# Kernel optimization log

Measured on AMD Instinct MI355X. Metric: run time of the kernel, lower is better.

Reference implementation:

```python
import jax, jax.numpy as jnp
import numpy as np

B, N, FEAT = 64, 1024, 3
HID, STATE, LAYERS, NTYPES = 64, 32, 2, 10


def setup_inputs() -> dict:
    key = jax.random.key(0)
    ks = jax.random.split(key, 16)
    s = 0.1
    return {
        "task_features": jax.random.normal(ks[0], (B, N, FEAT), jnp.float32),
        "task_types": jax.random.randint(ks[1], (B, N), 0, NTYPES, jnp.int32),
        "prev_state": jnp.zeros((B, STATE), jnp.float32),
        "enc_w1": jax.random.normal(ks[2], (HID, FEAT), jnp.float32) * s,
        "enc_b1": jnp.zeros((HID,), jnp.float32),
        "enc_w2": jax.random.normal(ks[3], (HID, HID), jnp.float32) * s,
        "enc_b2": jnp.zeros((HID,), jnp.float32),
        "contention": jax.random.normal(ks[4], (NTYPES, NTYPES), jnp.float32) * 0.1,
        "gnn_w": jax.random.normal(ks[5], (LAYERS, HID, HID), jnp.float32) * s,
        "gnn_b": jnp.zeros((LAYERS, HID), jnp.float32),
        "gru_w_ih": jax.random.normal(ks[6], (3 * STATE, HID), jnp.float32) * s,
        "gru_w_hh": jax.random.normal(ks[7], (3 * STATE, STATE), jnp.float32) * s,
        "gru_b_ih": jnp.zeros((3 * STATE,), jnp.float32),
        "gru_b_hh": jnp.zeros((3 * STATE,), jnp.float32),
        "head_w1": jax.random.normal(ks[8], (HID, HID + STATE), jnp.float32) * s,
        "head_b1": jnp.zeros((HID,), jnp.float32),
        "head_w2": jax.random.normal(ks[9], (1, HID), jnp.float32) * s,
        "head_b2": jnp.zeros((1,), jnp.float32),
    }


def _forward(task_features, task_types, prev_state, enc_w1, enc_b1, enc_w2, enc_b2,
             contention, gnn_w, gnn_b, gru_w_ih, gru_w_hh, gru_b_ih, gru_b_hh,
             head_w1, head_b1, head_w2, head_b2):
    # task encoder: Linear -> ReLU -> Linear
    emb = jax.nn.relu(task_features @ enc_w1.T + enc_b1) @ enc_w2.T + enc_b2  # (B,N,H)
    # interaction graph: type-pair gather + cosine similarity
    base = contention[task_types[:, :, None], task_types[:, None, :]]  # (B,N,N)
    nrm = emb / jnp.maximum(jnp.linalg.norm(emb, axis=-1, keepdims=True), 1e-12)
    sim = jnp.einsum("bnd,bmd->bnm", nrm, nrm)
    adjacency = jax.nn.sigmoid(base) * sim  # (B,N,N)
    # GNN layers: aggregate + linear + relu
    h = emb
    for l in range(LAYERS):
        agg = jnp.einsum("bnm,bmd->bnd", adjacency, h)
        h = jax.nn.relu((h + agg) @ gnn_w[l].T + gnn_b[l])
    ctx = h.mean(axis=1)  # (B,H)
    # GRUCell (torch semantics)
    gi = ctx @ gru_w_ih.T + gru_b_ih
    gh = prev_state @ gru_w_hh.T + gru_b_hh
    i_r, i_z, i_n = jnp.split(gi, 3, axis=-1)
    h_r, h_z, h_n = jnp.split(gh, 3, axis=-1)
    r = jax.nn.sigmoid(i_r + h_r)
    z = jax.nn.sigmoid(i_z + h_z)
    n = jnp.tanh(i_n + r * h_n)
    new_state = (1.0 - z) * n + z * prev_state  # (B,S)
    # latency head on [h, state]
    st = jnp.broadcast_to(new_state[:, None, :], (h.shape[0], h.shape[1], new_state.shape[-1]))
    combined = jnp.concatenate([h, st], axis=-1)
    lat = jax.nn.relu(combined @ head_w1.T + head_b1) @ head_w2.T + head_b2
    return lat[..., 0], new_state


def reference(task_features, task_types, prev_state, enc_w1, enc_b1, enc_w2, enc_b2,
              contention, gnn_w, gnn_b, gru_w_ih, gru_w_hh, gru_b_ih, gru_b_hh,
              head_w1, head_b1, head_w2, head_b2):
    return _forward(task_features, task_types, prev_state, enc_w1, enc_b1, enc_w2, enc_b2,
                    contention, gnn_w, gnn_b, gru_w_ih, gru_w_hh, gru_b_ih, gru_b_hh,
                    head_w1, head_b1, head_w2, head_b2)
```

## Files before the change

### kernel.cpp

```cpp
#include <hip/hip_runtime.h>
#include <math.h>

#define BB 64
#define NN 1024
#define HID 64
#define STATE 32
#define NTYPES 10

typedef _Float16 f16;
typedef f16 f16x8 __attribute__((ext_vector_type(8)));
typedef f16 f16x4 __attribute__((ext_vector_type(4)));
typedef float f32x4 __attribute__((ext_vector_type(4)));

#define MFMA16(a, b, c) __builtin_amdgcn_mfma_f32_16x16x32_f16(a, b, c, 0, 0, 0)

__device__ __forceinline__ float sigm(float x) { return 1.f / (1.f + expf(-x)); }

__device__ __forceinline__ f16x8 cvt8(float4 a, float4 b) {
    f16x8 r;
    r[0] = (f16)a.x; r[1] = (f16)a.y; r[2] = (f16)a.z; r[3] = (f16)a.w;
    r[4] = (f16)b.x; r[5] = (f16)b.y; r[6] = (f16)b.z; r[7] = (f16)b.w;
    return r;
}
__device__ __forceinline__ unsigned packh2(f16 a, f16 b) {
    union { f16 h[2]; unsigned u; } p;
    p.h[0] = a; p.h[1] = b;
    return p.u;
}

__global__ __launch_bounds__(256) void k_misc(
    const float* __restrict__ w2, const float* __restrict__ gw,
    const float* __restrict__ hw1, f16* __restrict__ out,
    int* __restrict__ cnt, float* __restrict__ ctx)
{
    int p = blockIdx.x * 256 + threadIdx.x;
    if (p < 18432) {
        const float* W; int K, pl;
        if (p < 12288) { int seg = p >> 12; pl = p & 4095; W = (seg == 0) ? w2 : gw + (seg - 1) * 4096; K = 64; }
        else { W = hw1; K = 96; pl = p - 12288; }
        int j = pl & 7, lane = (pl >> 3) & 63, nt = (pl >> 9) & 3, ch = pl >> 11;
        int k = ch * 32 + ((lane >> 4) << 3) + j;
        int o = nt * 16 + (lane & 15);
        out[p] = (f16)W[o * K + k];
        return;
    }
    int q = p - 18432;
    if (q < BB * NTYPES) { cnt[q] = 0; return; }
    q -= BB * NTYPES;
    if (q < BB * HID) ctx[q] = 0.f;
}

__global__ __launch_bounds__(256) void k_encoder(
    const float* __restrict__ feat,
    const float* __restrict__ w1, const float* __restrict__ b1,
    const f16* __restrict__ w2f, const float* __restrict__ b2,
    const int* __restrict__ types, int* __restrict__ idx, int* __restrict__ cnt,
    f16* __restrict__ nrm, float* __restrict__ sclv)
{
    __shared__ f16 w2s[4096];
    __shared__ f16 tmp[4][16 * 72];
    __shared__ float fbuf[4][48];
    int tid = threadIdx.x, wave = tid >> 6, lane = tid & 63;
    int l15 = lane & 15, quad = lane >> 4;
    if (tid < 64) {
        int row = blockIdx.x * 64 + tid;
        int b = row >> 10;
        int t = types[row];
        int pos = atomicAdd(&cnt[b * NTYPES + t], 1);
        idx[(b * NTYPES + t) * NN + pos] = row & (NN - 1);
    }
    { const uint4* s = (const uint4*)w2f; uint4* d = (uint4*)w2s;
      for (int i = tid; i < 512; i += 256) d[i] = s[i]; }
    float w10 = w1[lane * 3], w11 = w1[lane * 3 + 1], w12 = w1[lane * 3 + 2], b1l = b1[lane];
    int tb = blockIdx.x * 64 + wave * 16;
    if (lane < 48) fbuf[wave][lane] = feat[tb * 3 + lane];
    __syncthreads();
    f16* tw = &tmp[wave][0];
#pragma unroll
    for (int r = 0; r < 16; ++r) {
        float x0 = fbuf[wave][r * 3], x1 = fbuf[wave][r * 3 + 1], x2 = fbuf[wave][r * 3 + 2];
        float hv = fmaxf(fmaf(w10, x0, fmaf(w11, x1, fmaf(w12, x2, b1l))), 0.f);
        tw[r * 72 + lane] = (f16)hv;
    }
    __builtin_amdgcn_sched_barrier(0);
    f16x8 a0 = *(const f16x8*)&tw[l15 * 72 + quad * 8];
    f16x8 a1 = *(const f16x8*)&tw[l15 * 72 + 32 + quad * 8];
    const f16x8* bf = (const f16x8*)w2s;
    f32x4 acc[4];
#pragma unroll
    for (int nt = 0; nt < 4; ++nt) {
        f32x4 c = {0.f, 0.f, 0.f, 0.f};
        c = MFMA16(a0, bf[(0 * 4 + nt) * 64 + lane], c);
        c = MFMA16(a1, bf[(1 * 4 + nt) * 64 + lane], c);
        acc[nt] = c;
    }
    float b2c[4];
#pragma unroll
    for (int nt = 0; nt < 4; ++nt) b2c[nt] = b2[nt * 16 + l15];
#pragma unroll
    for (int i = 0; i < 4; ++i) {
        float v[4]; float ss = 0.f;
#pragma unroll
        for (int nt = 0; nt < 4; ++nt) { v[nt] = acc[nt][i] + b2c[nt]; ss = fmaf(v[nt], v[nt], ss); }
        ss += __shfl_xor(ss, 1, 64); ss += __shfl_xor(ss, 2, 64);
        ss += __shfl_xor(ss, 4, 64); ss += __shfl_xor(ss, 8, 64);
        float nm = fmaxf(sqrtf(ss), 1e-12f);
        float rinv = 1.f / nm;
        int grow = tb + quad * 4 + i;
#pragma unroll
        for (int nt = 0; nt < 4; ++nt)
            nrm[(size_t)grow * 64 + nt * 16 + l15] = (f16)(v[nt] * rinv);
        if (l15 == 0) sclv[grow] = nm;
    }
}

#define TSTR2 72
__global__ __launch_bounds__(256) void k_buildM(
    const int* __restrict__ idx, const int* __restrict__ cnt,
    const f16* __restrict__ nrm, const f16* __restrict__ h,
    const float* __restrict__ scale, f16* __restrict__ M)
{
    __shared__ f16 nT[64 * TSTR2];
    __shared__ f16 hT[64 * TSTR2];
    int bj = blockIdx.x;
    int b = bj / NTYPES;
    int c = cnt[bj];
    const int* lst = idx + (size_t)bj * NN;
    int tid = threadIdx.x, wave = tid >> 6, lane = tid & 63;
    int l15 = lane & 15, quad = lane >> 4;
    int r = tid & 15;
    int q4 = tid >> 4;
    const f16* nb = nrm + (size_t)b * NN * 64;
    const f16* hb = h + (size_t)b * NN * 64;
    const float* sb = scale ? scale + (size_t)b * NN : nullptr;
    f32x4 acc[4] = {{0.f,0.f,0.f,0.f},{0.f,0.f,0.f,0.f},{0.f,0.f,0.f,0.f},{0.f,0.f,0.f,0.f}};
    for (int k0 = 0; k0 < c; k0 += 64) {
        __syncthreads();
        f16x4 a[4], g[4];
#pragma unroll
        for (int u = 0; u < 4; ++u) { a[u] = (f16x4){0,0,0,0}; g[u] = (f16x4){0,0,0,0}; }
#pragma unroll
        for (int u = 0; u < 4; ++u) {
            int mi = k0 + 4 * r + u;
            if (mi < c) {
                int m = lst[mi];
                a[u] = *(const f16x4*)&nb[(size_t)m * 64 + 4 * q4];
                if (sb) { f16 sm = (f16)sb[m]; f16x4 sv = {sm, sm, sm, sm}; g[u] = a[u] * sv; }
                else g[u] = *(const f16x4*)&hb[(size_t)m * 64 + 4 * q4];
            }
        }
#pragma unroll
        for (int i = 0; i < 4; ++i) {
            *(unsigned*)&nT[(4 * q4 + i) * TSTR2 + 4 * r]     = packh2(a[0][i], a[1][i]);
            *(unsigned*)&nT[(4 * q4 + i) * TSTR2 + 4 * r + 2] = packh2(a[2][i], a[3][i]);
            *(unsigned*)&hT[(4 * q4 + i) * TSTR2 + 4 * r]     = packh2(g[0][i], g[1][i]);
            *(unsigned*)&hT[(4 * q4 + i) * TSTR2 + 4 * r + 2] = packh2(g[2][i], g[3][i]);
        }
        __syncthreads();
        f16x8 af0 = *(const f16x8*)&nT[(wave * 16 + l15) * TSTR2 + quad * 8];
        f16x8 af1 = *(const f16x8*)&nT[(wave * 16 + l15) * TSTR2 + 32 + quad * 8];
#pragma unroll
        for (int nt = 0; nt < 4; ++nt) {
            f16x8 bf0 = *(const f16x8*)&hT[(nt * 16 + l15) * TSTR2 + quad * 8];
            f16x8 bf1 = *(const f16x8*)&hT[(nt * 16 + l15) * TSTR2 + 32 + quad * 8];
            acc[nt] = MFMA16(af0, bf0, acc[nt]);
            acc[nt] = MFMA16(af1, bf1, acc[nt]);
        }
    }
    f16* Mo = M + (size_t)bj * 4096;
#pragma unroll
    for (int nt = 0; nt < 4; ++nt)
#pragma unroll
        for (int i = 0; i < 4; ++i)
            Mo[(wave * 16 + quad * 4 + i) * 64 + nt * 16 + l15] = (f16)acc[nt][i];
}

__global__ __launch_bounds__(256) void k_gnn_layer(
    const int* __restrict__ idx, const int* __restrict__ cnt,
    const float* __restrict__ cont, const f16* __restrict__ M,
    const f16* __restrict__ nrm, const f16* __restrict__ h,
    const float* __restrict__ scale,
    const f16* __restrict__ gwf, const float* __restrict__ gb,
    f16* __restrict__ hout, float* __restrict__ ctx)
{
    __shared__ f16 ds_[4096];
    __shared__ f16 gs[4096];
    int i0 = blockIdx.x;
    int xcd = i0 & 7, k = i0 >> 3;
    int b = xcd + 8 * (k / NTYPES);
    int t = k % NTYPES;
    int bt = b * NTYPES + t;
    int c = cnt[bt];
    if (c == 0) return;
    int tid = threadIdx.x, wave = tid >> 6, lane = tid & 63;
    int l15 = lane & 15, quad = lane >> 4;
    { const uint4* s2 = (const uint4*)gwf; uint4* d2 = (uint4*)gs;
      for (int i = tid; i < 512; i += 256) d2[i] = s2[i]; }
    float sg[NTYPES];
#pragma unroll
    for (int j = 0; j < NTYPES; ++j) sg[j] = sigm(cont[t * NTYPES + j]);
    float ca[16];
#pragma unroll
    for (int i = 0; i < 16; ++i) ca[i] = 0.f;
    const f16* Mb = M + (size_t)b * NTYPES * 4096;
#pragma unroll
    for (int j = 0; j < NTYPES; ++j) {
        const f16* Mr = Mb + j * 4096 + (wave * 16 + l15) * 64;
        f16x8 m0 = *(const f16x8*)&Mr[quad * 8];
        f16x8 m1 = *(const f16x8*)&Mr[32 + quad * 8];
        float sv = sg[j];
#pragma unroll
        for (int e = 0; e < 8; ++e) {
            ca[e]     = fmaf(sv, (float)m0[e], ca[e]);
            ca[8 + e] = fmaf(sv, (float)m1[e], ca[8 + e]);
        }
    }
    f16x8 ca0, ca1;
#pragma unroll
    for (int i = 0; i < 8; ++i) { ca0[i] = (f16)ca[i]; ca1[i] = (f16)ca[8 + i]; }
    __syncthreads();
    const f16x8* gbf = (const f16x8*)gs;
#pragma unroll
    for (int nt = 0; nt < 4; ++nt) {
        f32x4 dd = {0.f, 0.f, 0.f, 0.f};
        dd = MFMA16(ca0, gbf[(0 * 4 + nt) * 64 + lane], dd);
        dd = MFMA16(ca1, gbf[(1 * 4 + nt) * 64 + lane], dd);
#pragma unroll
        for (int i = 0; i < 4; ++i) {
            int d = wave * 16 + quad * 4 + i;
            int pos = (((d >> 5) * 4 + nt) * 64 + ((d >> 3) & 3) * 16 + l15) * 8 + (d & 7);
            ds_[pos] = (f16)dd[i];
        }
    }
    __syncthreads();
    float gbl[4];
#pragma unroll
    for (int nt = 0; nt < 4; ++nt) gbl[nt] = gb[nt * 16 + l15];
    const int* lst = idx + (size_t)bt * NN;
    const f16* nb = nrm + (size_t)b * NN * 64;
    const f16* hb = h + (size_t)b * NN * 64;
    const float* sb = scale ? scale + (size_t)b * NN : nullptr;
    f16* hob = hout + (size_t)b * NN * 64;
    const f16x8* dbf = (const f16x8*)ds_;
    float cacc[4] = {0.f, 0.f, 0.f, 0.f};
    for (int g = wave; g * 16 < c; g += 4) {
        int tb = g * 16;
        int rA = tb + l15; if (rA >= c) rA = c - 1;
        int mA = lst[rA];
        const f16* na = nb + (size_t)mA * 64;
        f16x8 a0 = *(const f16x8*)&na[quad * 8];
        f16x8 a1 = *(const f16x8*)&na[32 + quad * 8];
        if (sb) {
            f32x4 acc1[4], acc2[4];
#pragma unroll
            for (int nt = 0; nt < 4; ++nt) {
                f32x4 c1 = {0.f, 0.f, 0.f, 0.f}, c2 = {0.f, 0.f, 0.f, 0.f};
                c1 = MFMA16(a0, dbf[(0 * 4 + nt) * 64 + lane], c1);
                c1 = MFMA16(a1, dbf[(1 * 4 + nt) * 64 + lane], c1);
                c2 = MFMA16(a0, gbf[(0 * 4 + nt) * 64 + lane], c2);
                c2 = MFMA16(a1, gbf[(1 * 4 + nt) * 64 + lane], c2);
                acc1[nt] = c1; acc2[nt] = c2;
            }
#pragma unroll
            for (int i = 0; i < 4; ++i) {
                int rr = tb + quad * 4 + i;
                if (rr < c) {
                    int m = lst[rr];
                    float sm = sb[m];
#pragma unroll
                    for (int nt = 0; nt < 4; ++nt) {
                        float v = fmaxf(fmaf(sm, acc2[nt][i], acc1[nt][i]) + gbl[nt], 0.f);
                        hob[(size_t)m * 64 + nt * 16 + l15] = (f16)v;
                    }
                }
            }
        } else {
            const f16* ha = hb + (size_t)mA * 64;
            f16x8 h0 = *(const f16x8*)&ha[quad * 8];
            f16x8 h1 = *(const f16x8*)&ha[32 + quad * 8];
            f32x4 acc[4];
#pragma unroll
            for (int nt = 0; nt < 4; ++nt) {
                f32x4 cc = {0.f, 0.f, 0.f, 0.f};
                cc = MFMA16(a0, dbf[(0 * 4 + nt) * 64 + lane], cc);
                cc = MFMA16(a1, dbf[(1 * 4 + nt) * 64 + lane], cc);
                cc = MFMA16(h0, gbf[(0 * 4 + nt) * 64 + lane], cc);
                cc = MFMA16(h1, gbf[(1 * 4 + nt) * 64 + lane], cc);
                acc[nt] = cc;
            }
#pragma unroll
            for (int i = 0; i < 4; ++i) {
                int rr = tb + quad * 4 + i;
                if (rr < c) {
                    int m = lst[rr];
#pragma unroll
                    for (int nt = 0; nt < 4; ++nt) {
                        float v = fmaxf(acc[nt][i] + gbl[nt], 0.f);
                        hob[(size_t)m * 64 + nt * 16 + l15] = (f16)v;
                        cacc[nt] += v;
                    }
                }
            }
        }
    }
    if (ctx) {
#pragma unroll
        for (int nt = 0; nt < 4; ++nt) {
            float sv = cacc[nt];
            sv += __shfl_xor(sv, 16, 64);
            sv += __shfl_xor(sv, 32, 64);
            if (quad == 0) atomicAdd(&ctx[b * HID + nt * 16 + l15], sv);
        }
    }
}

__global__ __launch_bounds__(256) void k_head(
    const f16* __restrict__ h2, const float* __restrict__ ctx_sum,
    const float* __restrict__ prev,
    const float* __restrict__ w_ih, const float* __restrict__ w_hh,
    const float* __restrict__ b_ih, const float* __restrict__ b_hh,
    const f16* __restrict__ hwf, const float* __restrict__ b1,
    const float* __restrict__ w2, const float* __restrict__ b2,
    float* __restrict__ lat, float* __restrict__ state_out)
{
    __shared__ f16 ws_[6144];
    __shared__ __align__(16) float st[STATE];
    __shared__ float cs[HID], ps[STATE], gis[96], ghs[96];
    int tid = threadIdx.x, wave = tid >> 6, lane = tid & 63;
    int l15 = lane & 15, quad = lane >> 4;
    int b = blockIdx.x >> 4;
    { const uint4* s = (const uint4*)hwf; uint4* d = (uint4*)ws_;
      for (int i = tid; i < 768; i += 256) d[i] = s[i]; }
    if (tid < HID) cs[tid] = ctx_sum[b * HID + tid] * (1.f / NN);
    if (tid >= HID && tid < HID + STATE) ps[tid - HID] = prev[b * STATE + tid - HID];
    __syncthreads();
    if (tid < 96) {
        float gi = b_ih[tid];
#pragma unroll 8
        for (int k = 0; k < HID; ++k) gi = fmaf(w_ih[tid * HID + k], cs[k], gi);
        float gh = b_hh[tid];
#pragma unroll
        for (int k = 0; k < STATE; ++k) gh = fmaf(w_hh[tid * STATE + k], ps[k], gh);
        gis[tid] = gi; ghs[tid] = gh;
    }
    __syncthreads();
    if (tid < STATE) {
        float r = sigm(gis[tid] + ghs[tid]);
        float z = sigm(gis[32 + tid] + ghs[32 + tid]);
        float nn = tanhf(gis[64 + tid] + r * ghs[64 + tid]);
        float v = (1.f - z) * nn + z * ps[tid];
        st[tid] = v;
        if ((blockIdx.x & 15) == 0) state_out[b * STATE + tid] = v;
    }
    __syncthreads();
    float b1c[4], w2c[4];
#pragma unroll
    for (int nt = 0; nt < 4; ++nt) { b1c[nt] = b1[nt * 16 + l15]; w2c[nt] = w2[nt * 16 + l15]; }
    float b2v = b2[0];
    int tb = blockIdx.x * 64 + wave * 16;
    int grow = tb + l15;
    const f16* ha = h2 + (size_t)grow * 64;
    f16x8 a0 = *(const f16x8*)&ha[quad * 8];
    f16x8 a1 = *(const f16x8*)&ha[32 + quad * 8];
    const float4* sp = (const float4*)st;
    f16x8 a2 = cvt8(sp[quad * 2], sp[quad * 2 + 1]);
    const f16x8* bf = (const f16x8*)ws_;
    f32x4 acc[4];
#pragma unroll
    for (int nt = 0; nt < 4; ++nt) {
        f32x4 cc = {0.f, 0.f, 0.f, 0.f};
        cc = MFMA16(a0, bf[(0 * 4 + nt) * 64 + lane], cc);
        cc = MFMA16(a1, bf[(1 * 4 + nt) * 64 + lane], cc);
        cc = MFMA16(a2, bf[(2 * 4 + nt) * 64 + lane], cc);
        acc[nt] = cc;
    }
#pragma unroll
    for (int i = 0; i < 4; ++i) {
        float s = 0.f;
#pragma unroll
        for (int nt = 0; nt < 4; ++nt) s = fmaf(fmaxf(acc[nt][i] + b1c[nt], 0.f), w2c[nt], s);
        s += __shfl_xor(s, 1, 64); s += __shfl_xor(s, 2, 64);
        s += __shfl_xor(s, 4, 64); s += __shfl_xor(s, 8, 64);
        if (l15 == 0) lat[tb + quad * 4 + i] = s + b2v;
    }
}

extern "C" void kernel_launch(void* const* d_in, const int* in_sizes, int n_in,
                              void* d_out, int out_size, void* d_ws, size_t ws_size,
                              hipStream_t stream) {
    const float* feat   = (const float*)d_in[0];
    const int*   types  = (const int*)d_in[1];
    const float* prev   = (const float*)d_in[2];
    const float* enc_w1 = (const float*)d_in[3];
    const float* enc_b1 = (const float*)d_in[4];
    const float* enc_w2 = (const float*)d_in[5];
    const float* enc_b2 = (const float*)d_in[6];
    const float* cont   = (const float*)d_in[7];
    const float* gnn_w  = (const float*)d_in[8];
    const float* gnn_b  = (const float*)d_in[9];
    const float* w_ih   = (const float*)d_in[10];
    const float* w_hh   = (const float*)d_in[11];
    const float* b_ih   = (const float*)d_in[12];
    const float* b_hh   = (const float*)d_in[13];
    const float* hw1    = (const float*)d_in[14];
    const float* hb1    = (const float*)d_in[15];
    const float* hw2    = (const float*)d_in[16];
    const float* hb2    = (const float*)d_in[17];
    float* out = (float*)d_out;

    float* ws  = (float*)d_ws;
    f16*   nrm = (f16*)ws;
    f16*   h1  = (f16*)(ws + 2097152);
    f16*   h2  = (f16*)(ws + 4194304);
    float* scl = ws + 6291456;
    int*   idx = (int*)(ws + 6356992);
    int*   cnt = idx + BB * NTYPES * NN;
    f16*   M0  = (f16*)(ws + 7012992);
    f16*   M1  = (f16*)(ws + 8323712);
    f16*   wfrag = (f16*)(ws + 9634432);
    float* ctx   = ws + 9643648;
    f16*   w2f  = wfrag;
    f16*   gw0f = wfrag + 4096;
    f16*   gw1f = wfrag + 8192;
    f16*   hwf  = wfrag + 12288;

    k_misc<<<91, 256, 0, stream>>>(enc_w2, gnn_w, hw1, wfrag, cnt, ctx);
    k_encoder<<<BB * NN / 64, 256, 0, stream>>>(feat, enc_w1, enc_b1, w2f, enc_b2,
                                                types, idx, cnt, nrm, scl);
    k_buildM<<<BB * NTYPES, 256, 0, stream>>>(idx, cnt, nrm, nrm, scl, M0);
    k_gnn_layer<<<BB * NTYPES, 256, 0, stream>>>(idx, cnt, cont, M0, nrm, nrm, scl,
                                                 gw0f, gnn_b, h1, nullptr);
    k_buildM<<<BB * NTYPES, 256, 0, stream>>>(idx, cnt, nrm, h1, nullptr, M1);
    k_gnn_layer<<<BB * NTYPES, 256, 0, stream>>>(idx, cnt, cont, M1, nrm, h1, nullptr,
                                                 gw1f, gnn_b + HID, h2, ctx);
    k_head<<<BB * NN / 64, 256, 0, stream>>>(h2, ctx, prev, w_ih, w_hh, b_ih, b_hh,
                                             hwf, hb1, hw2, hb2, out, out + BB * NN);
}
```

Before: 180.7 us.

## Fuse first GNN layer with construction of the next layer's M matrix

Adds a kernel that computes layer-0 GNN outputs for each (batch, type) group and, in the same pass, accumulates the nrm^T·h1 product that k_buildM previously produced in a separate launch. This drops one kernel launch and the re-read of h1 and nrm from global memory. In exchange the fused kernel uses more shared memory for the transposed tiles and adds two barriers per 64-row chunk. The general k_gnn_layer is reduced to the non-scaled path only. Empty groups (c==0) no longer exit early, so they still write a zero M block.

```diff
diff --git a/kernel.cpp b/kernel.cpp
--- a/kernel.cpp
+++ b/kernel.cpp
@@ -175,6 +175,143 @@
             Mo[(wave * 16 + quad * 4 + i) * 64 + nt * 16 + l15] = (f16)acc[nt][i];
 }
 
+__global__ __launch_bounds__(256) void k_gnn0_fused(
+    const int* __restrict__ idx, const int* __restrict__ cnt,
+    const float* __restrict__ cont, const f16* __restrict__ M,
+    const f16* __restrict__ nrm, const float* __restrict__ scale,
+    const f16* __restrict__ gwf, const float* __restrict__ gb,
+    f16* __restrict__ hout, f16* __restrict__ Mout)
+{
+    __shared__ f16 ds_[4096];
+    __shared__ f16 gs[4096];
+    __shared__ __align__(16) f16 nT[64 * TSTR2];
+    __shared__ __align__(16) f16 hT[64 * TSTR2];
+    int i0 = blockIdx.x;
+    int xcd = i0 & 7, k = i0 >> 3;
+    int b = xcd + 8 * (k / NTYPES);
+    int t = k % NTYPES;
+    int bt = b * NTYPES + t;
+    int c = cnt[bt];
+    int tid = threadIdx.x, wave = tid >> 6, lane = tid & 63;
+    int l15 = lane & 15, quad = lane >> 4;
+    { const uint4* s2 = (const uint4*)gwf; uint4* d2 = (uint4*)gs;
+      for (int i = tid; i < 512; i += 256) d2[i] = s2[i]; }
+    float sg[NTYPES];
+#pragma unroll
+    for (int j = 0; j < NTYPES; ++j) sg[j] = sigm(cont[t * NTYPES + j]);
+    float ca[16];
+#pragma unroll
+    for (int i = 0; i < 16; ++i) ca[i] = 0.f;
+    const f16* Mb = M + (size_t)b * NTYPES * 4096;
+#pragma unroll
+    for (int j = 0; j < NTYPES; ++j) {
+        const f16* Mr = Mb + j * 4096 + (wave * 16 + l15) * 64;
+        f16x8 m0 = *(const f16x8*)&Mr[quad * 8];
+        f16x8 m1 = *(const f16x8*)&Mr[32 + quad * 8];
+        float sv = sg[j];
+#pragma unroll
+        for (int e = 0; e < 8; ++e) {
+            ca[e]     = fmaf(sv, (float)m0[e], ca[e]);
+            ca[8 + e] = fmaf(sv, (float)m1[e], ca[8 + e]);
+        }
+    }
+    f16x8 ca0, ca1;
+#pragma unroll
+    for (int i = 0; i < 8; ++i) { ca0[i] = (f16)ca[i]; ca1[i] = (f16)ca[8 + i]; }
+    __syncthreads();
+    const f16x8* gbf = (const f16x8*)gs;
+#pragma unroll
+    for (int nt = 0; nt < 4; ++nt) {
+        f32x4 dd = {0.f, 0.f, 0.f, 0.f};
+        dd = MFMA16(ca0, gbf[(0 * 4 + nt) * 64 + lane], dd);
+        dd = MFMA16(ca1, gbf[(1 * 4 + nt) * 64 + lane], dd);
+#pragma unroll
+        for (int i = 0; i < 4; ++i) {
+            int d = wave * 16 + quad * 4 + i;
+            int pos = (((d >> 5) * 4 + nt) * 64 + ((d >> 3) & 3) * 16 + l15) * 8 + (d & 7);
+            ds_[pos] = (f16)dd[i];
+        }
+    }
+    __syncthreads();
+    float gbl[4];
+#pragma unroll
+    for (int nt = 0; nt < 4; ++nt) gbl[nt] = gb[nt * 16 + l15];
+    const int* lst = idx + (size_t)bt * NN;
+    const f16* nb = nrm + (size_t)b * NN * 64;
+    const float* sb = scale + (size_t)b * NN;
+    f16* hob = hout + (size_t)b * NN * 64;
+    const f16x8* dbf = (const f16x8*)ds_;
+    f32x4 macc[4];
+#pragma unroll
+    for (int nt = 0; nt < 4; ++nt) macc[nt] = (f32x4){0.f, 0.f, 0.f, 0.f};
+    int nchunk = (c + 63) >> 6;
+    for (int ch = 0; ch < nchunk; ++ch) {
+        int tb = ch * 64 + wave * 16;
+        int rA = tb + l15;
+        bool okA = rA < c;
+        int mA = lst[okA ? rA : (c - 1)];
+        const f16* na = nb + (size_t)mA * 64;
+        f16x8 a0 = *(const f16x8*)&na[quad * 8];
+        f16x8 a1 = *(const f16x8*)&na[32 + quad * 8];
+        f32x4 acc1[4], acc2[4];
+#pragma unroll
+        for (int nt = 0; nt < 4; ++nt) {
+            f32x4 c1 = {0.f, 0.f, 0.f, 0.f}, c2 = {0.f, 0.f, 0.f, 0.f};
+            c1 = MFMA16(a0, dbf[(0 * 4 + nt) * 64 + lane], c1);
+            c1 = MFMA16(a1, dbf[(1 * 4 + nt) * 64 + lane], c1);
+            c2 = MFMA16(a0, gbf[(0 * 4 + nt) * 64 + lane], c2);
+            c2 = MFMA16(a1, gbf[(1 * 4 + nt) * 64 + lane], c2);
+            acc1[nt] = c1; acc2[nt] = c2;
+        }
+        f16x4 hv[4];
+#pragma unroll
+        for (int nt = 0; nt < 4; ++nt) hv[nt] = (f16x4){0, 0, 0, 0};
+#pragma unroll
+        for (int i = 0; i < 4; ++i) {
+            int rr = tb + quad * 4 + i;
+            if (rr < c) {
+                int m = lst[rr];
+                float sm = sb[m];
+#pragma unroll
+                for (int nt = 0; nt < 4; ++nt) {
+                    float v = fmaxf(fmaf(sm, acc2[nt][i], acc1[nt][i]) + gbl[nt], 0.f);
+                    f16 vh = (f16)v;
+                    hob[(size_t)m * 64 + nt * 16 + l15] = vh;
+                    hv[nt][i] = vh;
+                }
+            }
+        }
+        f16x8 z8 = {0, 0, 0, 0, 0, 0, 0, 0};
+        f16x8 s0 = okA ? a0 : z8;
+        f16x8 s1 = okA ? a1 : z8;
+#pragma unroll
+        for (int j = 0; j < 8; ++j) {
+            nT[(quad * 8 + j) * TSTR2 + wave * 16 + l15]      = s0[j];
+            nT[(32 + quad * 8 + j) * TSTR2 + wave * 16 + l15] = s1[j];
+        }
+#pragma unroll
+        for (int nt = 0; nt < 4; ++nt)
+            *(f16x4*)&hT[(nt * 16 + l15) * TSTR2 + wave * 16 + quad * 4] = hv[nt];
+        __syncthreads();
+        f16x8 af0 = *(const f16x8*)&nT[(wave * 16 + l15) * TSTR2 + quad * 8];
+        f16x8 af1 = *(const f16x8*)&nT[(wave * 16 + l15) * TSTR2 + 32 + quad * 8];
+#pragma unroll
+        for (int nt = 0; nt < 4; ++nt) {
+            f16x8 bf0 = *(const f16x8*)&hT[(nt * 16 + l15) * TSTR2 + quad * 8];
+            f16x8 bf1 = *(const f16x8*)&hT[(nt * 16 + l15) * TSTR2 + 32 + quad * 8];
+            macc[nt] = MFMA16(af0, bf0, macc[nt]);
+            macc[nt] = MFMA16(af1, bf1, macc[nt]);
+        }
+        __syncthreads();
+    }
+    f16* Mo = Mout + (size_t)bt * 4096;
+#pragma unroll
+    for (int nt = 0; nt < 4; ++nt)
+#pragma unroll
+        for (int i = 0; i < 4; ++i)
+            Mo[(wave * 16 + quad * 4 + i) * 64 + nt * 16 + l15] = (f16)macc[nt][i];
+}
+
 __global__ __launch_bounds__(256) void k_gnn_layer(
     const int* __restrict__ idx, const int* __restrict__ cnt,
     const float* __restrict__ cont, const f16* __restrict__ M,
@@ -239,7 +376,6 @@
     const int* lst = idx + (size_t)bt * NN;
     const f16* nb = nrm + (size_t)b * NN * 64;
     const f16* hb = h + (size_t)b * NN * 64;
-    const float* sb = scale ? scale + (size_t)b * NN : nullptr;
     f16* hob = hout + (size_t)b * NN * 64;
     const f16x8* dbf = (const f16x8*)ds_;
     float cacc[4] = {0.f, 0.f, 0.f, 0.f};
@@ -250,55 +386,29 @@
         const f16* na = nb + (size_t)mA * 64;
         f16x8 a0 = *(const f16x8*)&na[quad * 8];
         f16x8 a1 = *(const f16x8*)&na[32 + quad * 8];
-        if (sb) {
-            f32x4 acc1[4], acc2[4];
-#pragma unroll
-            for (int nt = 0; nt < 4; ++nt) {
-                f32x4 c1 = {0.f, 0.f, 0.f, 0.f}, c2 = {0.f, 0.f, 0.f, 0.f};
-                c1 = MFMA16(a0, dbf[(0 * 4 + nt) * 64 + lane], c1);
-                c1 = MFMA16(a1, dbf[(1 * 4 + nt) * 64 + lane], c1);
-                c2 = MFMA16(a0, gbf[(0 * 4 + nt) * 64 + lane], c2);
-                c2 = MFMA16(a1, gbf[(1 * 4 + nt) * 64 + lane], c2);
-                acc1[nt] = c1; acc2[nt] = c2;
-            }
-#pragma unroll
-            for (int i = 0; i < 4; ++i) {
-                int rr = tb + quad * 4 + i;
-                if (rr < c) {
-                    int m = lst[rr];
-                    float sm = sb[m];
-#pragma unroll
-                    for (int nt = 0; nt < 4; ++nt) {
-                        float v = fmaxf(fmaf(sm, acc2[nt][i], acc1[nt][i]) + gbl[nt], 0.f);
-                        hob[(size_t)m * 64 + nt * 16 + l15] = (f16)v;
-                    }
-                }
-            }
-        } else {
-            const f16* ha = hb + (size_t)mA * 64;
-            f16x8 h0 = *(const f16x8*)&ha[quad * 8];
-            f16x8 h1 = *(const f16x8*)&ha[32 + quad * 8];
-            f32x4 acc[4];
-#pragma unroll
-            for (int nt = 0; nt < 4; ++nt) {
-                f32x4 cc = {0.f, 0.f, 0.f, 0.f};
-                cc = MFMA16(a0, dbf[(0 * 4 + nt) * 64 + lane], cc);
-                cc = MFMA16(a1, dbf[(1 * 4 + nt) * 64 + lane], cc);
-                cc = MFMA16(h0, gbf[(0 * 4 + nt) * 64 + lane], cc);
-                cc = MFMA16(h1, gbf[(1 * 4 + nt) * 64 + lane], cc);
-                acc[nt] = cc;
-            }
-#pragma unroll
-            for (int i = 0; i < 4; ++i) {
-                int rr = tb + quad * 4 + i;
-                if (rr < c) {
-                    int m = lst[rr];
-#pragma unroll
-                    for (int nt = 0; nt < 4; ++nt) {
-                        float v = fmaxf(acc[nt][i] + gbl[nt], 0.f);
-                        hob[(size_t)m * 64 + nt * 16 + l15] = (f16)v;
-                        cacc[nt] += v;
-                    }
+        const f16* ha = hb + (size_t)mA * 64;
+        f16x8 h0 = *(const f16x8*)&ha[quad * 8];
+        f16x8 h1 = *(const f16x8*)&ha[32 + quad * 8];
+        f32x4 acc[4];
+#pragma unroll
+        for (int nt = 0; nt < 4; ++nt) {
+            f32x4 cc = {0.f, 0.f, 0.f, 0.f};
+            cc = MFMA16(a0, dbf[(0 * 4 + nt) * 64 + lane], cc);
+            cc = MFMA16(a1, dbf[(1 * 4 + nt) * 64 + lane], cc);
+            cc = MFMA16(h0, gbf[(0 * 4 + nt) * 64 + lane], cc);
+            cc = MFMA16(h1, gbf[(1 * 4 + nt) * 64 + lane], cc);
+            acc[nt] = cc;
+        }
+#pragma unroll
+        for (int i = 0; i < 4; ++i) {
+            int rr = tb + quad * 4 + i;
+            if (rr < c) {
+                int m = lst[rr];
+#pragma unroll
+                for (int nt = 0; nt < 4; ++nt) {
+                    float v = fmaxf(acc[nt][i] + gbl[nt], 0.f);
+                    hob[(size_t)m * 64 + nt * 16 + l15] = (f16)v;
+                    cacc[nt] += v;
                 }
             }
         }
@@ -428,9 +538,8 @@
     k_encoder<<<BB * NN / 64, 256, 0, stream>>>(feat, enc_w1, enc_b1, w2f, enc_b2,
                                                 types, idx, cnt, nrm, scl);
     k_buildM<<<BB * NTYPES, 256, 0, stream>>>(idx, cnt, nrm, nrm, scl, M0);
-    k_gnn_layer<<<BB * NTYPES, 256, 0, stream>>>(idx, cnt, cont, M0, nrm, nrm, scl,
-                                                 gw0f, gnn_b, h1, nullptr);
-    k_buildM<<<BB * NTYPES, 256, 0, stream>>>(idx, cnt, nrm, h1, nullptr, M1);
+    k_gnn0_fused<<<BB * NTYPES, 256, 0, stream>>>(idx, cnt, cont, M0, nrm, scl,
+                                                  gw0f, gnn_b, h1, M1);
     k_gnn_layer<<<BB * NTYPES, 256, 0, stream>>>(idx, cnt, cont, M1, nrm, h1, nullptr,
                                                  gw1f, gnn_b + HID, h2, ctx);
     k_head<<<BB * NN / 64, 256, 0, stream>>>(h2, ctx, prev, w_ih, w_hh, b_ih, b_hh,
```

After: 169.1 us. 6.4% less time.
